# Kernel optimization log

Hardware: AMD Instinct MI355X
Metric: run time of the kernel (lower is better)

Reference implementation:

```python
import jax, jax.numpy as jnp
import numpy as np

EPS_COS = 1e-8   # torch cosine_similarity norm clamp
EPS_IN = 1e-5    # InstanceNorm2d eps
MODALITY = 4


def setup_inputs() -> dict:
    key = jax.random.key(0)
    k1, k2 = jax.random.split(key)
    x = jax.random.normal(k1, (16, 256, 128, 128), dtype=jnp.float32)
    conv_w = jax.random.normal(k2, (64, 256), dtype=jnp.float32) * 0.05
    return {"x": x, "conv_w": conv_w}


def reference(x, conv_w):
    B, c, h, w = x.shape
    # (B, 4, N): each modality flattened over (c/4, h, w)
    xr = x.reshape(B, MODALITY, -1)
    norms = jnp.maximum(jnp.linalg.norm(xr, axis=-1), EPS_COS)  # (B,4)
    xn = xr / norms[:, :, None]
    # pairwise cosine similarity across modalities: (B,4,4)
    matrix = jnp.einsum('bin,bjn->bij', xn, xn) - jnp.eye(MODALITY, dtype=x.dtype)
    attention_score = -jnp.sum(matrix, axis=-1)                 # (B,4)
    attention_prob = jax.nn.softmax(attention_score, axis=-1)   # (B,4)
    # weight each modality's channels
    fused = (x.reshape(B, MODALITY, c // MODALITY, h, w)
             * attention_prob[:, :, None, None, None]).reshape(B, c, h, w)
    # 1x1 conv (no bias)
    y = jnp.einsum('bchw,oc->bohw', fused, conv_w)
    # InstanceNorm2d (affine=False): normalize over (h,w) per (b,o)
    mean = jnp.mean(y, axis=(2, 3), keepdims=True)
    var = jnp.mean(jnp.square(y - mean), axis=(2, 3), keepdims=True)
    y = (y - mean) / jnp.sqrt(var + EPS_IN)
    return jax.nn.relu(y)
```

## Files before the change

kernel.cpp:

```cpp
#include <hip/hip_runtime.h>
#include <hip/hip_bf16.h>

#define HW 16384
#define NC 256
#define NO 64
#define NPM 1048576
#define EPS_IN 1e-5f
#define DBLK 1024
#define WIN 1024
#define SPX 256
#define SCH 32
#define NCHK 8
#define PAD 4

typedef float f32x4 __attribute__((ext_vector_type(4)));
typedef short bhalf8 __attribute__((ext_vector_type(8)));

static __device__ __forceinline__ short f2bf(float f){
  __bf16 h = (__bf16)f;
  return __builtin_bit_cast(short, h);
}


__global__ void k_dots(const float* __restrict__ x, float* __restrict__ partials){
  __shared__ float lds[4][WIN];
  __shared__ float red[4][16];
  const int b = blockIdx.y, bx = blockIdx.x;
  const int tid = threadIdx.x;
  const int w = tid >> 6, lane = tid & 63;
  const int wi = (bx + b*67) & (DBLK-1);
  const float* src = x + (size_t)b*4*NPM + (size_t)w*NPM + (size_t)wi*WIN + lane*4;

  #pragma unroll
  for (int li=0; li<4; li++){
    __builtin_amdgcn_global_load_lds(
        (const __attribute__((address_space(1))) void*)(src + li*256),
        (__attribute__((address_space(3))) void*)&lds[w][li*256],
        16, 0, 0);
  }
  __syncthreads();

  float4 vv[4];
  #pragma unroll
  for (int m=0;m<4;m++) vv[m] = *(const float4*)&lds[m][tid*4];
  float acc[10];
  int k=0;
  #pragma unroll
  for (int i=0;i<4;i++)
    #pragma unroll
    for (int j=i;j<4;j++,k++)
      acc[k] = vv[i].x*vv[j].x + vv[i].y*vv[j].y + vv[i].z*vv[j].z + vv[i].w*vv[j].w;

  #pragma unroll
  for (int kk=0;kk<10;kk++){
    float s = acc[kk];
    #pragma unroll
    for (int off=1; off<64; off<<=1) s += __shfl_xor(s, off, 64);
    acc[kk]=s;
  }
  if (lane==0){
    #pragma unroll
    for (int kk=0;kk<10;kk++) red[w][kk] = acc[kk];
  }
  __syncthreads();
  if (tid<10){
    float s = red[0][tid] + red[1][tid] + red[2][tid] + red[3][tid];
    partials[((size_t)b*DBLK + bx)*10 + tid] = s;
  }
}

__global__ void k_attn(const float* __restrict__ partials, float* __restrict__ probs){
  __shared__ float red[4][16];
  int b = blockIdx.x, tid = threadIdx.x;
  int w = tid>>6, lane = tid&63;
  float a[10];
  #pragma unroll
  for (int kk=0;kk<10;kk++) a[kk]=0.f;
  #pragma unroll
  for (int r=0;r<DBLK/256;r++){
    const float* p = partials + ((size_t)b*DBLK + r*256 + tid)*10;
    #pragma unroll
    for (int kk=0;kk<10;kk++) a[kk]+=p[kk];
  }
  #pragma unroll
  for (int kk=0;kk<10;kk++){
    float s=a[kk];
    #pragma unroll
    for (int off=1;off<64;off<<=1) s+=__shfl_xor(s,off,64);
    a[kk]=s;
  }
  if (lane==0){
    #pragma unroll
    for (int kk=0;kk<10;kk++) red[w][kk]=a[kk];
  }
  __syncthreads();
  if (tid==0){
    float d[10];
    #pragma unroll
    for (int kk=0;kk<10;kk++) d[kk]=red[0][kk]+red[1][kk]+red[2][kk]+red[3][kk];
    float D[4][4];
    int k2=0;
    #pragma unroll
    for (int i=0;i<4;i++)
      #pragma unroll
      for (int j=i;j<4;j++,k2++){ D[i][j]=d[k2]; D[j][i]=d[k2]; }
    float nrm[4];
    #pragma unroll
    for (int m=0;m<4;m++) nrm[m]=fmaxf(sqrtf(D[m][m]),1e-8f);
    float sc[4];
    #pragma unroll
    for (int i=0;i<4;i++){
      float s=0.f;
      #pragma unroll
      for (int j=0;j<4;j++) s += D[i][j]/(nrm[i]*nrm[j]);
      sc[i] = -(s-1.0f);
    }
    float mx = fmaxf(fmaxf(sc[0],sc[1]), fmaxf(sc[2],sc[3]));
    float e[4], se=0.f;
    #pragma unroll
    for (int m=0;m<4;m++){ e[m]=expf(sc[m]-mx); se+=e[m]; }
    #pragma unroll
    for (int m=0;m<4;m++) probs[b*4+m]=e[m]/se;
  }
}

__launch_bounds__(256, 2)
__global__ void k_gemm(const float* __restrict__ x, const float* __restrict__ w,
                       const float* __restrict__ ws, float* __restrict__ y,
                       float* __restrict__ part){
  __shared__ float buf[2][SCH][SPX+PAD];
  const int b   = blockIdx.y;
  const int pw  = blockIdx.x * SPX;
  const int tid = threadIdx.x;
  const int wid = tid >> 6;
  const int lane = tid & 63;
  const int l15 = lane & 15;
  const int lg  = lane >> 4;
  const int wr  = wid & 1;
  const int wp  = wid >> 1;

  const float* probs = ws + 256 + b*4;
  float pm[4] = {probs[0], probs[1], probs[2], probs[3]};
  bhalf8 afrag[2][NCHK];
  const float4* w4 = reinterpret_cast<const float4*>(w);
  #pragma unroll
  for (int rt=0; rt<2; rt++){
    int row = wr*32 + rt*16 + l15;
    #pragma unroll
    for (int ks=0; ks<NCHK; ks++){
      float s = pm[ks>>1];
      float4 a0 = w4[row*64 + ks*8 + lg];
      float4 a1 = w4[row*64 + ks*8 + lg + 4];
      bhalf8 f;
      f[0]=f2bf(a0.x*s); f[1]=f2bf(a0.y*s); f[2]=f2bf(a0.z*s); f[3]=f2bf(a0.w*s);
      f[4]=f2bf(a1.x*s); f[5]=f2bf(a1.y*s); f[6]=f2bf(a1.z*s); f[7]=f2bf(a1.w*s);
      afrag[rt][ks] = f;
    }
  }

  const float* xb = x + (size_t)b*NC*HW + pw;

  auto STAGE = [&](int cc, int cur){
    #pragma unroll
    for (int j=0; j<8; j++){
      int ch_l = wid*8 + j;
      __builtin_amdgcn_global_load_lds(
          (const __attribute__((address_space(1))) void*)(xb + (size_t)(cc*SCH + ch_l)*HW + lane*4),
          (__attribute__((address_space(3))) void*)&buf[cur][ch_l][0],
          16, 0, 0);
    }
  };

  f32x4 acc[2][8];
  #pragma unroll
  for (int rt=0; rt<2; rt++)
    #pragma unroll
    for (int pt=0; pt<8; pt++) acc[rt][pt] = (f32x4){0.f,0.f,0.f,0.f};

  STAGE(0, 0);
  int cur = 0;
  #pragma unroll 1
  for (int cc=0; cc<NCHK; cc++){
    if (cc < NCHK-1){
      STAGE(cc+1, cur^1);
      asm volatile("s_waitcnt vmcnt(8)" ::: "memory");
    } else {
      asm volatile("s_waitcnt vmcnt(0)" ::: "memory");
    }
    __builtin_amdgcn_s_barrier();
    __builtin_amdgcn_sched_barrier(0);

    const float (*bp)[SPX+PAD] = buf[cur];
    #pragma unroll
    for (int pt=0; pt<8; pt++){
      int px_l = wp*128 + pt*16 + l15;
      bhalf8 bfr;
      #pragma unroll
      for (int eh=0; eh<2; eh++)
        #pragma unroll
        for (int el=0; el<4; el++){
          int c_l = lg*4 + el + eh*16;
          bfr[eh*4+el] = f2bf(bp[c_l][px_l]);
        }
      #pragma unroll
      for (int rt=0; rt<2; rt++)
        acc[rt][pt] = __builtin_amdgcn_mfma_f32_16x16x32_bf16(afrag[rt][cc], bfr, acc[rt][pt], 0, 0, 0);
    }

    __builtin_amdgcn_sched_barrier(0);
    __builtin_amdgcn_s_barrier();
    cur ^= 1;
  }

  float sacc[2][4] = {{0}}, qacc[2][4] = {{0}};
  #pragma unroll
  for (int rt=0; rt<2; rt++){
    #pragma unroll
    for (int pt=0; pt<8; pt++){
      size_t ybase = ((size_t)(b*NO + wr*32 + rt*16 + lg*4))*HW + pw + wp*128 + pt*16 + l15;
      #pragma unroll
      for (int r=0; r<4; r++){
        float v = acc[rt][pt][r];
        __builtin_nontemporal_store(v, &y[ybase + (size_t)r*HW]);
        sacc[rt][r] += v;
        qacc[rt][r] += v*v;
      }
    }
  }
  float* sp = part + ((size_t)(b*64 + blockIdx.x))*NO*4;
  #pragma unroll
  for (int rt=0; rt<2; rt++){
    #pragma unroll
    for (int r=0; r<4; r++){
      float s = sacc[rt][r], q = qacc[rt][r];
      #pragma unroll
      for (int off=1; off<16; off<<=1){
        s += __shfl_xor(s, off, 64);
        q += __shfl_xor(q, off, 64);
      }
      if (l15 == 0){
        int o = wr*32 + rt*16 + lg*4 + r;
        sp[o*4 + wp*2]     = s;
        sp[o*4 + wp*2 + 1] = q;
      }
    }
  }
}

__global__ void k_norm(float* __restrict__ y, const float* __restrict__ part){
  __shared__ float red2[2][2];
  const int bo = blockIdx.x, b = bo >> 6, o = bo & 63;
  const int tid = threadIdx.x;
  float s = 0.f, q = 0.f;
  if (tid < 128){
    int bx = tid >> 1, wp = tid & 1;
    const float* p = part + (((size_t)(b*64 + bx))*NO + o)*4 + wp*2;
    s = p[0]; q = p[1];
  }
  #pragma unroll
  for (int off=1; off<64; off<<=1){
    s += __shfl_xor(s, off, 64);
    q += __shfl_xor(q, off, 64);
  }
  if (tid < 128 && (tid & 63) == 0){ red2[tid>>6][0] = s; red2[tid>>6][1] = q; }
  __syncthreads();
  float S = red2[0][0] + red2[1][0];
  float Q = red2[0][1] + red2[1][1];
  float mean = S * (1.f/HW);
  float var  = Q * (1.f/HW) - mean*mean;
  float inv  = rsqrtf(var + EPS_IN);
  f32x4* yp = reinterpret_cast<f32x4*>(y) + (size_t)bo*(HW/4);
  #pragma unroll 4
  for (int i = tid; i < HW/4; i += 256){
    f32x4 v = yp[i];
    v.x = fmaxf((v.x-mean)*inv, 0.f);
    v.y = fmaxf((v.y-mean)*inv, 0.f);
    v.z = fmaxf((v.z-mean)*inv, 0.f);
    v.w = fmaxf((v.w-mean)*inv, 0.f);
    __builtin_nontemporal_store(v, &yp[i]);
  }
}

extern "C" void kernel_launch(void* const* d_in, const int* in_sizes, int n_in,
                              void* d_out, int out_size, void* d_ws, size_t ws_size,
                              hipStream_t stream){
  const float* x = (const float*)d_in[0];
  const float* w = (const float*)d_in[1];
  float* out = (float*)d_out;
  float* ws  = (float*)d_ws;
  float* partials = ws + 8192;
  float* probs    = ws + 256;
  float* part     = ws + 180224;

  k_dots<<<dim3(DBLK,16),    dim3(256), 0, stream>>>(x, partials);
  k_attn<<<dim3(16),         dim3(256), 0, stream>>>(partials, probs);
  k_gemm<<<dim3(HW/SPX,16),  dim3(256), 0, stream>>>(x, w, ws, out, part);
  k_norm<<<dim3(1024),       dim3(256), 0, stream>>>(out, part);
}
```

Baseline: 173.1 us.

## Halve GEMM pixel tile to 128 with two-wave blocks and paired-channel LDS rows

Shrinks the k_gemm block from 256 pixels with four waves to 128 pixels with two waves, each wave owning 32 output rows across all 128 pixels. The LDS staging is rearranged so each global_load_lds fills one padded row holding two channels of 128 pixels, which keeps the 16-byte-per-lane loads with half the pixel width. The grid doubles to 2048 blocks, meant to improve occupancy and load balance across CUs. Fewer waves per block are left to hide latency, each block does less work, and the norm partials layout changes to match.

```diff
diff --git a/kernel.cpp b/kernel.cpp
--- a/kernel.cpp
+++ b/kernel.cpp
@@ -8,10 +8,9 @@
 #define EPS_IN 1e-5f
 #define DBLK 1024
 #define WIN 1024
-#define SPX 256
-#define SCH 32
-#define NCHK 8
-#define PAD 4
+#define SPX 128
+#define NPR 16
+#define PRW 264
 
 typedef float f32x4 __attribute__((ext_vector_type(4)));
 typedef short bhalf8 __attribute__((ext_vector_type(8)));
@@ -124,11 +123,11 @@
   }
 }
 
-__launch_bounds__(256, 2)
+__launch_bounds__(128, 2)
 __global__ void k_gemm(const float* __restrict__ x, const float* __restrict__ w,
                        const float* __restrict__ ws, float* __restrict__ y,
                        float* __restrict__ part){
-  __shared__ float buf[2][SCH][SPX+PAD];
+  __shared__ float buf[2][NPR][PRW];
   const int b   = blockIdx.y;
   const int pw  = blockIdx.x * SPX;
   const int tid = threadIdx.x;
@@ -136,18 +135,16 @@
   const int lane = tid & 63;
   const int l15 = lane & 15;
   const int lg  = lane >> 4;
-  const int wr  = wid & 1;
-  const int wp  = wid >> 1;
 
   const float* probs = ws + 256 + b*4;
   float pm[4] = {probs[0], probs[1], probs[2], probs[3]};
-  bhalf8 afrag[2][NCHK];
+  bhalf8 afrag[2][8];
   const float4* w4 = reinterpret_cast<const float4*>(w);
   #pragma unroll
   for (int rt=0; rt<2; rt++){
-    int row = wr*32 + rt*16 + l15;
-    #pragma unroll
-    for (int ks=0; ks<NCHK; ks++){
+    int row = wid*32 + rt*16 + l15;
+    #pragma unroll
+    for (int ks=0; ks<8; ks++){
       float s = pm[ks>>1];
       float4 a0 = w4[row*64 + ks*8 + lg];
       float4 a1 = w4[row*64 + ks*8 + lg + 4];
@@ -163,10 +160,11 @@
   auto STAGE = [&](int cc, int cur){
     #pragma unroll
     for (int j=0; j<8; j++){
-      int ch_l = wid*8 + j;
+      int pr = wid*8 + j;
+      const float* src = xb + (size_t)(cc*32 + pr*2 + (lane>>5))*HW + (lane&31)*4;
       __builtin_amdgcn_global_load_lds(
-          (const __attribute__((address_space(1))) void*)(xb + (size_t)(cc*SCH + ch_l)*HW + lane*4),
-          (__attribute__((address_space(3))) void*)&buf[cur][ch_l][0],
+          (const __attribute__((address_space(1))) void*)src,
+          (__attribute__((address_space(3))) void*)&buf[cur][pr][0],
           16, 0, 0);
     }
   };
@@ -180,8 +178,8 @@
   STAGE(0, 0);
   int cur = 0;
   #pragma unroll 1
-  for (int cc=0; cc<NCHK; cc++){
-    if (cc < NCHK-1){
+  for (int cc=0; cc<8; cc++){
+    if (cc < 7){
       STAGE(cc+1, cur^1);
       asm volatile("s_waitcnt vmcnt(8)" ::: "memory");
     } else {
@@ -190,17 +188,17 @@
     __builtin_amdgcn_s_barrier();
     __builtin_amdgcn_sched_barrier(0);
 
-    const float (*bp)[SPX+PAD] = buf[cur];
+    const float (*bp)[PRW] = buf[cur];
     #pragma unroll
     for (int pt=0; pt<8; pt++){
-      int px_l = wp*128 + pt*16 + l15;
+      int px = pt*16 + l15;
       bhalf8 bfr;
       #pragma unroll
       for (int eh=0; eh<2; eh++)
         #pragma unroll
         for (int el=0; el<4; el++){
-          int c_l = lg*4 + el + eh*16;
-          bfr[eh*4+el] = f2bf(bp[c_l][px_l]);
+          int c = lg*4 + el + eh*16;
+          bfr[eh*4+el] = f2bf(bp[c>>1][(c&1)*128 + px]);
         }
       #pragma unroll
       for (int rt=0; rt<2; rt++)
@@ -217,7 +215,7 @@
   for (int rt=0; rt<2; rt++){
     #pragma unroll
     for (int pt=0; pt<8; pt++){
-      size_t ybase = ((size_t)(b*NO + wr*32 + rt*16 + lg*4))*HW + pw + wp*128 + pt*16 + l15;
+      size_t ybase = ((size_t)(b*NO + wid*32 + rt*16 + lg*4))*HW + pw + pt*16 + l15;
       #pragma unroll
       for (int r=0; r<4; r++){
         float v = acc[rt][pt][r];
@@ -227,7 +225,7 @@
       }
     }
   }
-  float* sp = part + ((size_t)(b*64 + blockIdx.x))*NO*4;
+  float* sp = part + ((size_t)(b*128 + blockIdx.x))*NO*2;
   #pragma unroll
   for (int rt=0; rt<2; rt++){
     #pragma unroll
@@ -239,9 +237,9 @@
         q += __shfl_xor(q, off, 64);
       }
       if (l15 == 0){
-        int o = wr*32 + rt*16 + lg*4 + r;
-        sp[o*4 + wp*2]     = s;
-        sp[o*4 + wp*2 + 1] = q;
+        int o = wid*32 + rt*16 + lg*4 + r;
+        sp[o*2]     = s;
+        sp[o*2 + 1] = q;
       }
     }
   }
@@ -253,8 +251,7 @@
   const int tid = threadIdx.x;
   float s = 0.f, q = 0.f;
   if (tid < 128){
-    int bx = tid >> 1, wp = tid & 1;
-    const float* p = part + (((size_t)(b*64 + bx))*NO + o)*4 + wp*2;
+    const float* p = part + (((size_t)(b*128 + tid))*NO + o)*2;
     s = p[0]; q = p[1];
   }
   #pragma unroll
@@ -294,6 +291,6 @@
 
   k_dots<<<dim3(DBLK,16),    dim3(256), 0, stream>>>(x, partials);
   k_attn<<<dim3(16),         dim3(256), 0, stream>>>(partials, probs);
-  k_gemm<<<dim3(HW/SPX,16),  dim3(256), 0, stream>>>(x, w, ws, out, part);
+  k_gemm<<<dim3(HW/SPX,16),  dim3(128), 0, stream>>>(x, w, ws, out, part);
   k_norm<<<dim3(1024),       dim3(256), 0, stream>>>(out, part);
 }
```

Measured after the change: 174.6 us. About the same (+0.9%).
